# Kernel tuning notes

Measured on AMD Instinct MI355X. Metric: run time of the kernel, lower is better.

The kernel has to match this reference:

```python
import jax, jax.numpy as jnp
import numpy as np

N, D, E = 50000, 64, 800000  # nodes, node_dim, edges


def setup_inputs() -> dict:
    key = jax.random.key(0)
    ks = jax.random.split(key, 9)
    def lin(kw, fan_in, fan_out):
        # torch nn.Linear default init: U(-1/sqrt(fan_in), 1/sqrt(fan_in))
        bound = 1.0 / np.sqrt(fan_in)
        kw1, kw2 = jax.random.split(kw)
        W = jax.random.uniform(kw1, (fan_in, fan_out), jnp.float32, -bound, bound)
        b = jax.random.uniform(kw2, (fan_out,), jnp.float32, -bound, bound)
        return W, b
    W1, b1 = lin(ks[0], 2 * D + 2, D)
    W2, b2 = lin(ks[1], D, D // 2)
    W3, b3 = lin(ks[2], D // 2, D // 4)
    return {
        "node_features": jax.random.normal(ks[3], (N, D), jnp.float32),
        "edge_index": jax.random.randint(ks[4], (2, E), 0, N, jnp.int64),
        "spatial_features": jax.random.normal(ks[5], (E, 2), jnp.float32),
        "W1": W1, "b1": b1, "W2": W2, "b2": b2, "W3": W3, "b3": b3,
    }


def reference(node_features, edge_index, spatial_features, W1, b1, W2, b2, W3, b3):
    src = node_features[edge_index[0]]          # [E, D] gather
    dst = node_features[edge_index[1]]          # [E, D] gather
    x = jnp.concatenate([src, dst, spatial_features], axis=1)  # [E, 2D+2]
    h = jax.nn.relu(x @ W1 + b1)                # [E, D]
    h = jax.nn.relu(h @ W2 + b2)                # [E, D//2]
    return h @ W3 + b3                          # [E, D//4]
```

## Files before the change

kernel.cpp:

```cpp
#include <hip/hip_runtime.h>
#include <hip/hip_bf16.h>

#define NE 800000
#define NN 50000
#define TPW 4
#define NTILES (NE / 16)
#define NODE_TILES (NN / 16)

typedef __attribute__((ext_vector_type(8))) short        s16x8;
typedef __attribute__((ext_vector_type(8))) __bf16       bf16x8;
typedef __attribute__((ext_vector_type(4))) float        f32x4;
typedef __attribute__((ext_vector_type(2))) float        f32x2;
typedef __attribute__((ext_vector_type(4))) unsigned int u32x4;
typedef __attribute__((ext_vector_type(2))) unsigned int u32x2;

#define TAB_OFF 16384
#define WS_TAB ((size_t)(TAB_OFF + 2ull * NN * 64) * 2)
#define WS_NFB ((size_t)(TAB_OFF + 1ull * NN * 64) * 2)

__device__ __forceinline__ unsigned short f2bf_bits(float f) {
    __bf16 b = (__bf16)f;
    return __builtin_bit_cast(unsigned short, b);
}

__device__ __forceinline__ unsigned int pkbf(float a, float b) {
    return (unsigned int)f2bf_bits(a) | ((unsigned int)f2bf_bits(b) << 16);
}

__device__ __forceinline__ s16x8 cvt8(f32x4 a, f32x4 b) {
    bf16x8 r;
    r[0] = (__bf16)a[0]; r[1] = (__bf16)a[1]; r[2] = (__bf16)a[2]; r[3] = (__bf16)a[3];
    r[4] = (__bf16)b[0]; r[5] = (__bf16)b[1]; r[6] = (__bf16)b[2]; r[7] = (__bf16)b[3];
    return __builtin_bit_cast(s16x8, r);
}

__device__ __forceinline__ void ubf2(unsigned int u, float& lo, float& hi) {
    lo = __builtin_bit_cast(float, u << 16);
    hi = __builtin_bit_cast(float, u & 0xFFFF0000u);
}

__global__ void prep(const float* __restrict__ W1, const float* __restrict__ W2,
                     const float* __restrict__ W3, const float* __restrict__ nf,
                     unsigned short* __restrict__ ws, int do_nf) {
    unsigned short* w1t = ws;
    unsigned short* w2t = ws + 10240;
    unsigned short* w3t = ws + 12288;
    int t = blockIdx.x * blockDim.x + threadIdx.x;
    int stride = gridDim.x * blockDim.x;
    for (int i = t; i < 64 * 160; i += stride) {
        int j = i / 160, k = i % 160;
        w1t[i] = f2bf_bits(k < 130 ? W1[k * 64 + j] : 0.0f);
    }
    for (int i = t; i < 32 * 64; i += stride) {
        int j = i / 64, k = i % 64;
        w2t[i] = f2bf_bits(W2[k * 32 + j]);
    }
    for (int i = t; i < 16 * 32; i += stride) {
        int j = i / 32, k = i % 32;
        w3t[i] = f2bf_bits(W3[k * 16 + j]);
    }
    if (do_nf) {
        unsigned short* nfb = ws + TAB_OFF;
        for (int i = t; i < NN * 8; i += stride) {
            f32x4 a = *reinterpret_cast<const f32x4*>(nf + (long)i * 8);
            f32x4 b = *reinterpret_cast<const f32x4*>(nf + (long)i * 8 + 4);
            *reinterpret_cast<s16x8*>(nfb + (long)i * 8) = cvt8(a, b);
        }
    }
}

__global__ __launch_bounds__(256) void node_prep(
    const float* __restrict__ nf, const unsigned short* __restrict__ wsw,
    unsigned short* __restrict__ At, unsigned short* __restrict__ Bt) {
    const unsigned short* w1t = wsw;
    const int tid = threadIdx.x, wid = tid >> 6, lane = tid & 63;
    const int lr = lane & 15, lg = lane >> 4;

    s16x8 w1f[4][4];
    #pragma unroll
    for (int s = 0; s < 4; ++s)
        #pragma unroll
        for (int c = 0; c < 4; ++c)
            w1f[s][c] = *reinterpret_cast<const s16x8*>(w1t + (c * 16 + lr) * 160 + s * 32 + lg * 8);

    for (int tile = blockIdx.x * 4 + wid; tile < NODE_TILES; tile += gridDim.x * 4) {
        const int row = tile * 16 + lr;
        const float* p = nf + (long)row * 64;
        s16x8 nfr[2];
        #pragma unroll
        for (int s = 0; s < 2; ++s) {
            f32x4 a = *reinterpret_cast<const f32x4*>(p + s * 32 + lg * 8);
            f32x4 b = *reinterpret_cast<const f32x4*>(p + s * 32 + lg * 8 + 4);
            nfr[s] = cvt8(a, b);
        }
        f32x4 a4[4], b4[4];
        #pragma unroll
        for (int c = 0; c < 4; ++c) { a4[c] = (f32x4){0,0,0,0}; b4[c] = (f32x4){0,0,0,0}; }
        #pragma unroll
        for (int s = 0; s < 2; ++s)
            #pragma unroll
            for (int c = 0; c < 4; ++c) {
                a4[c] = __builtin_amdgcn_mfma_f32_16x16x32_bf16(w1f[s][c],     nfr[s], a4[c], 0, 0, 0);
                b4[c] = __builtin_amdgcn_mfma_f32_16x16x32_bf16(w1f[s + 2][c], nfr[s], b4[c], 0, 0, 0);
            }
        #pragma unroll
        for (int c = 0; c < 4; ++c) {
            u32x2 pa, pb;
            pa[0] = pkbf(a4[c][0], a4[c][1]); pa[1] = pkbf(a4[c][2], a4[c][3]);
            pb[0] = pkbf(b4[c][0], b4[c][1]); pb[1] = pkbf(b4[c][2], b4[c][3]);
            *reinterpret_cast<u32x2*>(At + (long)row * 64 + c * 16 + lg * 4) = pa;
            *reinterpret_cast<u32x2*>(Bt + (long)row * 64 + c * 16 + lg * 4) = pb;
        }
    }
}

__device__ __forceinline__ void gatherT(const unsigned short* At, const unsigned short* Bt,
                                        int si, int di, int lg, s16x8 g[4]) {
    const unsigned short* pa = At + (size_t)si * 64 + lg * 8;
    const unsigned short* pb = Bt + (size_t)di * 64 + lg * 8;
    g[0] = *reinterpret_cast<const s16x8*>(pa);
    g[1] = *reinterpret_cast<const s16x8*>(pa + 32);
    g[2] = *reinterpret_cast<const s16x8*>(pb);
    g[3] = *reinterpret_cast<const s16x8*>(pb + 32);
}

__global__ __launch_bounds__(256) void edge_mlp_tab(
    const int* __restrict__ ei, const float* __restrict__ sp,
    const float* __restrict__ W1, const float* __restrict__ b1,
    const float* __restrict__ b2, const float* __restrict__ b3,
    const unsigned short* __restrict__ wsw, float* __restrict__ out) {

    const unsigned short* w2t = wsw + 10240;
    const unsigned short* w3t = wsw + 12288;
    const unsigned short* At  = wsw + TAB_OFF;
    const unsigned short* Bt  = At + (size_t)NN * 64;

    __shared__ unsigned short h2s[4 * 16 * 40];

    const int tid = threadIdx.x, wid = tid >> 6, lane = tid & 63;
    const int lr = lane & 15, lg = lane >> 4;

    s16x8 w2f[2][2], w3f;
    #pragma unroll
    for (int s = 0; s < 2; ++s)
        #pragma unroll
        for (int c = 0; c < 2; ++c)
            w2f[s][c] = *reinterpret_cast<const s16x8*>(w2t + (c * 16 + lr) * 64 + s * 32 + lg * 8);
    w3f = *reinterpret_cast<const s16x8*>(w3t + lr * 32 + lg * 8);

    f32x4 b2v[2];
    #pragma unroll
    for (int c = 0; c < 2; ++c) b2v[c] = *reinterpret_cast<const f32x4*>(b2 + c * 16 + lg * 4);
    const f32x4 b3v = *reinterpret_cast<const f32x4*>(b3 + lg * 4);

    float c0f[2][8], c1f[2][8], cbf[2][8];
    #pragma unroll
    for (int jb = 0; jb < 2; ++jb) {
        const int j0 = jb * 32 + lg * 8;
        *reinterpret_cast<f32x4*>(&c0f[jb][0]) = *reinterpret_cast<const f32x4*>(W1 + 128 * 64 + j0);
        *reinterpret_cast<f32x4*>(&c0f[jb][4]) = *reinterpret_cast<const f32x4*>(W1 + 128 * 64 + j0 + 4);
        *reinterpret_cast<f32x4*>(&c1f[jb][0]) = *reinterpret_cast<const f32x4*>(W1 + 129 * 64 + j0);
        *reinterpret_cast<f32x4*>(&c1f[jb][4]) = *reinterpret_cast<const f32x4*>(W1 + 129 * 64 + j0 + 4);
        *reinterpret_cast<f32x4*>(&cbf[jb][0]) = *reinterpret_cast<const f32x4*>(b1 + j0);
        *reinterpret_cast<f32x4*>(&cbf[jb][4]) = *reinterpret_cast<const f32x4*>(b1 + j0 + 4);
    }

    const int tile0 = (blockIdx.x * 4 + wid) * TPW;
    int si[TPW], di[TPW];
    f32x2 spv[TPW];
    #pragma unroll
    for (int t = 0; t < TPW; ++t) {
        const int e = (tile0 + t) * 16 + lr;
        si[t] = ei[e];
        di[t] = ei[NE + e];
        spv[t] = *reinterpret_cast<const f32x2*>(sp + 2 * (size_t)e);
    }

    unsigned short* h2w = h2s + wid * (16 * 40) + lr * 40;

    s16x8 cur[4], nxt[4];
    gatherT(At, Bt, si[0], di[0], lg, cur);

    #pragma unroll
    for (int tt = 0; tt < TPW; ++tt) {
        if (tt + 1 < TPW)
            gatherT(At, Bt, si[tt + 1], di[tt + 1], lg, nxt);

        const float sp0 = spv[tt][0], sp1 = spv[tt][1];

        s16x8 bfr[2];
        #pragma unroll
        for (int jb = 0; jb < 2; ++jb) {
            u32x4 au = __builtin_bit_cast(u32x4, cur[jb]);
            u32x4 bu = __builtin_bit_cast(u32x4, cur[2 + jb]);
            u32x4 pk4;
            #pragma unroll
            for (int q = 0; q < 4; ++q) {
                float alo, ahi, blo, bhi;
                ubf2(au[q], alo, ahi);
                ubf2(bu[q], blo, bhi);
                float h0 = fmaf(sp0, c0f[jb][2 * q],
                           fmaf(sp1, c1f[jb][2 * q],     cbf[jb][2 * q]     + (alo + blo)));
                float h1 = fmaf(sp0, c0f[jb][2 * q + 1],
                           fmaf(sp1, c1f[jb][2 * q + 1], cbf[jb][2 * q + 1] + (ahi + bhi)));
                pk4[q] = pkbf(fmaxf(h0, 0.f), fmaxf(h1, 0.f));
            }
            bfr[jb] = __builtin_bit_cast(s16x8, pk4);
        }

        f32x4 acc2[2];
        #pragma unroll
        for (int c = 0; c < 2; ++c) acc2[c] = (f32x4){0, 0, 0, 0};
        #pragma unroll
        for (int s = 0; s < 2; ++s)
            #pragma unroll
            for (int c = 0; c < 2; ++c)
                acc2[c] = __builtin_amdgcn_mfma_f32_16x16x32_bf16(w2f[s][c], bfr[s], acc2[c], 0, 0, 0);

        #pragma unroll
        for (int c = 0; c < 2; ++c) {
            u32x2 p;
            p[0] = pkbf(fmaxf(acc2[c][0] + b2v[c][0], 0.f), fmaxf(acc2[c][1] + b2v[c][1], 0.f));
            p[1] = pkbf(fmaxf(acc2[c][2] + b2v[c][2], 0.f), fmaxf(acc2[c][3] + b2v[c][3], 0.f));
            *reinterpret_cast<u32x2*>(h2w + c * 16 + lg * 4) = p;
        }

        s16x8 bf3 = *reinterpret_cast<const s16x8*>(h2w + lg * 8);
        f32x4 acc3 = (f32x4){0, 0, 0, 0};
        acc3 = __builtin_amdgcn_mfma_f32_16x16x32_bf16(w3f, bf3, acc3, 0, 0, 0);

        f32x4 o;
        #pragma unroll
        for (int r = 0; r < 4; ++r) o[r] = acc3[r] + b3v[r];
        __builtin_nontemporal_store(o,
            reinterpret_cast<f32x4*>(out + (long)((tile0 + tt) * 16 + lr) * 16 + lg * 4));

        #pragma unroll
        for (int s = 0; s < 4; ++s) cur[s] = nxt[s];
    }
}

template <bool BF16NF>
__device__ __forceinline__ void gather4(const unsigned short* nfb, const float* nf,
                                        int si, int di, int lg, s16x8 g[4]) {
    if (BF16NF) {
        #pragma unroll
        for (int s = 0; s < 4; ++s) {
            const int row = (s < 2) ? si : di;
            g[s] = *reinterpret_cast<const s16x8*>(nfb + (long)row * 64 + (s & 1) * 32 + lg * 8);
        }
    } else {
        #pragma unroll
        for (int s = 0; s < 4; ++s) {
            const float* p = nf + (long)((s < 2) ? si : di) * 64 + (s & 1) * 32 + lg * 8;
            f32x4 a = *reinterpret_cast<const f32x4*>(p);
            f32x4 b = *reinterpret_cast<const f32x4*>(p + 4);
            g[s] = cvt8(a, b);
        }
    }
}

template <bool BF16NF>
__global__ __launch_bounds__(256) void edge_mlp_fb(
    const float* __restrict__ nf, const int* __restrict__ ei,
    const float* __restrict__ sp, const float* __restrict__ b1,
    const float* __restrict__ b2, const float* __restrict__ b3,
    const unsigned short* __restrict__ wsw, float* __restrict__ out) {

    const unsigned short* w1t = wsw;
    const unsigned short* w2t = wsw + 10240;
    const unsigned short* w3t = wsw + 12288;
    const unsigned short* nfb = wsw + TAB_OFF;

    __shared__ float h1s[4][16][68];
    __shared__ float h2s[4][16][36];

    const int tid = threadIdx.x, wid = tid >> 6, lane = tid & 63;
    const int lr = lane & 15, lg = lane >> 4;

    s16x8 w1f[5][4], w2f[2][2], w3f;
    #pragma unroll
    for (int s = 0; s < 5; ++s)
        #pragma unroll
        for (int c = 0; c < 4; ++c)
            w1f[s][c] = *reinterpret_cast<const s16x8*>(w1t + (c * 16 + lr) * 160 + s * 32 + lg * 8);
    #pragma unroll
    for (int s = 0; s < 2; ++s)
        #pragma unroll
        for (int c = 0; c < 2; ++c)
            w2f[s][c] = *reinterpret_cast<const s16x8*>(w2t + (c * 16 + lr) * 64 + s * 32 + lg * 8);
    w3f = *reinterpret_cast<const s16x8*>(w3t + lr * 32 + lg * 8);

    float bias1[4], bias2[2], bias3;
    #pragma unroll
    for (int c = 0; c < 4; ++c) bias1[c] = b1[c * 16 + lr];
    #pragma unroll
    for (int c = 0; c < 2; ++c) bias2[c] = b2[c * 16 + lr];
    bias3 = b3[lr];

    const int tile0 = (blockIdx.x * 4 + wid) * TPW;
    int si[TPW], di[TPW];
    f32x2 spv[TPW];
    #pragma unroll
    for (int t = 0; t < TPW; ++t) {
        const int e = (tile0 + t) * 16 + lr;
        si[t] = ei[e];
        di[t] = ei[NE + e];
        spv[t] = *reinterpret_cast<const f32x2*>(sp + 2 * (size_t)e);
    }

    s16x8 cur[4], nxt[4];
    gather4<BF16NF>(nfb, nf, si[0], di[0], lg, cur);

    #pragma unroll
    for (int tt = 0; tt < TPW; ++tt) {
        if (tt + 1 < TPW)
            gather4<BF16NF>(nfb, nf, si[tt + 1], di[tt + 1], lg, nxt);

        const int ebase = (tile0 + tt) * 16;

        f32x4 acc1[4];
        #pragma unroll
        for (int c = 0; c < 4; ++c) acc1[c] = (f32x4){0, 0, 0, 0};
        #pragma unroll
        for (int s = 0; s < 4; ++s)
            #pragma unroll
            for (int c = 0; c < 4; ++c)
                acc1[c] = __builtin_amdgcn_mfma_f32_16x16x32_bf16(cur[s], w1f[s][c], acc1[c], 0, 0, 0);
        {
            bf16x8 z;
            #pragma unroll
            for (int j = 0; j < 8; ++j) z[j] = (__bf16)0.0f;
            if (lg == 0) { z[0] = (__bf16)spv[tt][0]; z[1] = (__bf16)spv[tt][1]; }
            s16x8 af = __builtin_bit_cast(s16x8, z);
            #pragma unroll
            for (int c = 0; c < 4; ++c)
                acc1[c] = __builtin_amdgcn_mfma_f32_16x16x32_bf16(af, w1f[4][c], acc1[c], 0, 0, 0);
        }
        #pragma unroll
        for (int c = 0; c < 4; ++c)
            #pragma unroll
            for (int r = 0; r < 4; ++r)
                h1s[wid][lg * 4 + r][c * 16 + lr] = fmaxf(acc1[c][r] + bias1[c], 0.0f);

        f32x4 acc2[2];
        #pragma unroll
        for (int c = 0; c < 2; ++c) acc2[c] = (f32x4){0, 0, 0, 0};
        #pragma unroll
        for (int s = 0; s < 2; ++s) {
            f32x4 a = *reinterpret_cast<const f32x4*>(&h1s[wid][lr][s * 32 + lg * 8]);
            f32x4 b = *reinterpret_cast<const f32x4*>(&h1s[wid][lr][s * 32 + lg * 8 + 4]);
            s16x8 af = cvt8(a, b);
            #pragma unroll
            for (int c = 0; c < 2; ++c)
                acc2[c] = __builtin_amdgcn_mfma_f32_16x16x32_bf16(af, w2f[s][c], acc2[c], 0, 0, 0);
        }
        #pragma unroll
        for (int c = 0; c < 2; ++c)
            #pragma unroll
            for (int r = 0; r < 4; ++r)
                h2s[wid][lg * 4 + r][c * 16 + lr] = fmaxf(acc2[c][r] + bias2[c], 0.0f);

        f32x4 a3 = *reinterpret_cast<const f32x4*>(&h2s[wid][lr][lg * 8]);
        f32x4 b3x = *reinterpret_cast<const f32x4*>(&h2s[wid][lr][lg * 8 + 4]);
        s16x8 af3 = cvt8(a3, b3x);
        f32x4 acc3 = (f32x4){0, 0, 0, 0};
        acc3 = __builtin_amdgcn_mfma_f32_16x16x32_bf16(af3, w3f, acc3, 0, 0, 0);
        #pragma unroll
        for (int r = 0; r < 4; ++r)
            out[(long)(ebase + lg * 4 + r) * 16 + lr] = acc3[r] + bias3;

        #pragma unroll
        for (int s = 0; s < 4; ++s) cur[s] = nxt[s];
    }
}

extern "C" void kernel_launch(void* const* d_in, const int* in_sizes, int n_in,
                              void* d_out, int out_size, void* d_ws, size_t ws_size,
                              hipStream_t stream) {
    const float* nf = (const float*)d_in[0];
    const int*   ei = (const int*)d_in[1];
    const float* sp = (const float*)d_in[2];
    const float* W1 = (const float*)d_in[3];
    const float* b1 = (const float*)d_in[4];
    const float* W2 = (const float*)d_in[5];
    const float* b2 = (const float*)d_in[6];
    const float* W3 = (const float*)d_in[7];
    const float* b3 = (const float*)d_in[8];
    float* out = (float*)d_out;
    unsigned short* wsw = (unsigned short*)d_ws;

    const bool tab  = (ws_size >= WS_TAB);
    const bool bnfb = (!tab && ws_size >= WS_NFB);

    hipLaunchKernelGGL(prep, dim3(64), dim3(256), 0, stream,
                       W1, W2, W3, nf, wsw, bnfb ? 1 : 0);

    const int blocks = NTILES / TPW / 4;
    if (tab) {
        hipLaunchKernelGGL(node_prep, dim3(196), dim3(256), 0, stream,
                           nf, wsw, wsw + TAB_OFF, wsw + TAB_OFF + (size_t)NN * 64);
        hipLaunchKernelGGL(edge_mlp_tab, dim3(blocks), dim3(256), 0, stream,
                           ei, sp, W1, b1, b2, b3, wsw, out);
    } else if (bnfb) {
        hipLaunchKernelGGL(edge_mlp_fb<true>, dim3(blocks), dim3(256), 0, stream,
                           nf, ei, sp, b1, b2, b3, wsw, out);
    } else {
        hipLaunchKernelGGL(edge_mlp_fb<false>, dim3(blocks), dim3(256), 0, stream,
                           nf, ei, sp, b1, b2, b3, wsw, out);
    }
}
```

Baseline: 65.85 us.

## Fuse weight prep into node table kernel, fold bias, double-buffer edge index loads

The default table path drops the separate prep launch. The node-table kernel now reads and converts W1 fragments directly, and block 0 also transposes W2/W3. The layer-1 bias is folded into the source-node table, which removes a per-edge add. The edge kernel processes 8 tiles per wave with double-buffered index/spatial loads, nontemporal index loads, packed f32x2 math and alternating LDS scratch buffers. This saves one launch and some per-edge work, at the cost of fewer waves and more registers, plus a race risk because W2/W3 are written by block 0 in the same kernel but read only by the next kernel.

Result: slower. 77.59 us (+17.8%).

```diff
diff --git a/kernel.cpp b/kernel.cpp
--- a/kernel.cpp
+++ b/kernel.cpp
@@ -3,7 +3,7 @@
 
 #define NE 800000
 #define NN 50000
-#define TPW 4
+#define TPW 8
 #define NTILES (NE / 16)
 #define NODE_TILES (NN / 16)
 
@@ -34,9 +34,230 @@
     return __builtin_bit_cast(s16x8, r);
 }
 
-__device__ __forceinline__ void ubf2(unsigned int u, float& lo, float& hi) {
-    lo = __builtin_bit_cast(float, u << 16);
-    hi = __builtin_bit_cast(float, u & 0xFFFF0000u);
+__global__ __launch_bounds__(256) void node_prep_all(
+    const float* __restrict__ nf, const float* __restrict__ W1,
+    const float* __restrict__ b1, const float* __restrict__ W2,
+    const float* __restrict__ W3, unsigned short* __restrict__ ws) {
+    unsigned short* w2t = ws + 10240;
+    unsigned short* w3t = ws + 12288;
+    unsigned short* At  = ws + TAB_OFF;
+    unsigned short* Bt  = At + (size_t)NN * 64;
+
+    const int tid = threadIdx.x, wid = tid >> 6, lane = tid & 63;
+    const int lr = lane & 15, lg = lane >> 4;
+
+    if (blockIdx.x == 0) {
+        for (int i = tid; i < 32 * 64; i += 256) {
+            int j = i / 64, k = i % 64;
+            w2t[i] = f2bf_bits(W2[k * 32 + j]);
+        }
+        for (int i = tid; i < 16 * 32; i += 256) {
+            int j = i / 32, k = i % 32;
+            w3t[i] = f2bf_bits(W3[k * 16 + j]);
+        }
+    }
+
+    s16x8 w1f[4][4];
+    #pragma unroll
+    for (int s = 0; s < 4; ++s)
+        #pragma unroll
+        for (int c = 0; c < 4; ++c) {
+            bf16x8 w;
+            #pragma unroll
+            for (int b = 0; b < 8; ++b)
+                w[b] = (__bf16)W1[(s * 32 + lg * 8 + b) * 64 + c * 16 + lr];
+            w1f[s][c] = __builtin_bit_cast(s16x8, w);
+        }
+
+    f32x4 b1q[4];
+    #pragma unroll
+    for (int c = 0; c < 4; ++c)
+        b1q[c] = *reinterpret_cast<const f32x4*>(b1 + c * 16 + lg * 4);
+
+    for (int tile = blockIdx.x * 4 + wid; tile < NODE_TILES; tile += gridDim.x * 4) {
+        const int row = tile * 16 + lr;
+        const float* p = nf + (long)row * 64;
+        s16x8 nfr[2];
+        #pragma unroll
+        for (int s = 0; s < 2; ++s) {
+            f32x4 a = *reinterpret_cast<const f32x4*>(p + s * 32 + lg * 8);
+            f32x4 b = *reinterpret_cast<const f32x4*>(p + s * 32 + lg * 8 + 4);
+            nfr[s] = cvt8(a, b);
+        }
+        f32x4 a4[4], b4[4];
+        #pragma unroll
+        for (int c = 0; c < 4; ++c) { a4[c] = (f32x4){0,0,0,0}; b4[c] = (f32x4){0,0,0,0}; }
+        #pragma unroll
+        for (int s = 0; s < 2; ++s)
+            #pragma unroll
+            for (int c = 0; c < 4; ++c) {
+                a4[c] = __builtin_amdgcn_mfma_f32_16x16x32_bf16(w1f[s][c],     nfr[s], a4[c], 0, 0, 0);
+                b4[c] = __builtin_amdgcn_mfma_f32_16x16x32_bf16(w1f[s + 2][c], nfr[s], b4[c], 0, 0, 0);
+            }
+        #pragma unroll
+        for (int c = 0; c < 4; ++c) {
+            u32x2 pa, pb;
+            pa[0] = pkbf(a4[c][0] + b1q[c][0], a4[c][1] + b1q[c][1]);
+            pa[1] = pkbf(a4[c][2] + b1q[c][2], a4[c][3] + b1q[c][3]);
+            pb[0] = pkbf(b4[c][0], b4[c][1]);
+            pb[1] = pkbf(b4[c][2], b4[c][3]);
+            *reinterpret_cast<u32x2*>(At + (long)row * 64 + c * 16 + lg * 4) = pa;
+            *reinterpret_cast<u32x2*>(Bt + (long)row * 64 + c * 16 + lg * 4) = pb;
+        }
+    }
+}
+
+__device__ __forceinline__ void gatherT(const unsigned short* At, const unsigned short* Bt,
+                                        int si, int di, int lg, s16x8 g[4]) {
+    const unsigned short* pa = At + (size_t)si * 64 + lg * 8;
+    const unsigned short* pb = Bt + (size_t)di * 64 + lg * 8;
+    g[0] = *reinterpret_cast<const s16x8*>(pa);
+    g[1] = *reinterpret_cast<const s16x8*>(pa + 32);
+    g[2] = *reinterpret_cast<const s16x8*>(pb);
+    g[3] = *reinterpret_cast<const s16x8*>(pb + 32);
+}
+
+__device__ __forceinline__ void compute_tile(
+    int tile, const s16x8 cur[4], f32x2 s2,
+    const f32x2 c0p[2][4], const f32x2 c1p[2][4],
+    const s16x8 w2f[2][2], s16x8 w3f,
+    const f32x4 b2v[2], f32x4 b3v,
+    unsigned short* h2w, int lg, int lr, float* __restrict__ out) {
+
+    const f32x2 sp0v = {s2[0], s2[0]}, sp1v = {s2[1], s2[1]};
+
+    s16x8 bfr[2];
+    #pragma unroll
+    for (int jb = 0; jb < 2; ++jb) {
+        u32x4 au = __builtin_bit_cast(u32x4, cur[jb]);
+        u32x4 bu = __builtin_bit_cast(u32x4, cur[2 + jb]);
+        u32x4 pk4;
+        #pragma unroll
+        for (int q = 0; q < 4; ++q) {
+            f32x2 av = {__builtin_bit_cast(float, au[q] << 16),
+                        __builtin_bit_cast(float, au[q] & 0xFFFF0000u)};
+            f32x2 bv = {__builtin_bit_cast(float, bu[q] << 16),
+                        __builtin_bit_cast(float, bu[q] & 0xFFFF0000u)};
+            f32x2 h = av + bv;
+            h = sp1v * c1p[jb][q] + h;
+            h = sp0v * c0p[jb][q] + h;
+            pk4[q] = pkbf(fmaxf(h[0], 0.f), fmaxf(h[1], 0.f));
+        }
+        bfr[jb] = __builtin_bit_cast(s16x8, pk4);
+    }
+
+    f32x4 acc2[2];
+    #pragma unroll
+    for (int c = 0; c < 2; ++c) acc2[c] = (f32x4){0, 0, 0, 0};
+    #pragma unroll
+    for (int s = 0; s < 2; ++s)
+        #pragma unroll
+        for (int c = 0; c < 2; ++c)
+            acc2[c] = __builtin_amdgcn_mfma_f32_16x16x32_bf16(w2f[s][c], bfr[s], acc2[c], 0, 0, 0);
+
+    #pragma unroll
+    for (int c = 0; c < 2; ++c) {
+        u32x2 p;
+        p[0] = pkbf(fmaxf(acc2[c][0] + b2v[c][0], 0.f), fmaxf(acc2[c][1] + b2v[c][1], 0.f));
+        p[1] = pkbf(fmaxf(acc2[c][2] + b2v[c][2], 0.f), fmaxf(acc2[c][3] + b2v[c][3], 0.f));
+        *reinterpret_cast<u32x2*>(h2w + c * 16 + lg * 4) = p;
+    }
+
+    s16x8 bf3 = *reinterpret_cast<const s16x8*>(h2w + lg * 8);
+    f32x4 acc3 = (f32x4){0, 0, 0, 0};
+    acc3 = __builtin_amdgcn_mfma_f32_16x16x32_bf16(w3f, bf3, acc3, 0, 0, 0);
+
+    f32x4 o;
+    #pragma unroll
+    for (int r = 0; r < 4; ++r) o[r] = acc3[r] + b3v[r];
+    __builtin_nontemporal_store(o,
+        reinterpret_cast<f32x4*>(out + (long)(tile * 16 + lr) * 16 + lg * 4));
+}
+
+__global__ __launch_bounds__(256) void edge_mlp_tab(
+    const int* __restrict__ ei, const float* __restrict__ sp,
+    const float* __restrict__ W1, const float* __restrict__ b2,
+    const float* __restrict__ b3, const unsigned short* __restrict__ wsw,
+    float* __restrict__ out) {
+
+    const unsigned short* w2t = wsw + 10240;
+    const unsigned short* w3t = wsw + 12288;
+    const unsigned short* At  = wsw + TAB_OFF;
+    const unsigned short* Bt  = At + (size_t)NN * 64;
+
+    __shared__ unsigned short h2s[2][4 * 16 * 40];
+
+    const int tid = threadIdx.x, wid = tid >> 6, lane = tid & 63;
+    const int lr = lane & 15, lg = lane >> 4;
+
+    const int wgid  = blockIdx.x * 4 + wid;
+    const int tile0 = wgid * TPW;
+    if (tile0 >= NTILES) return;
+
+    s16x8 w2f[2][2], w3f;
+    #pragma unroll
+    for (int s = 0; s < 2; ++s)
+        #pragma unroll
+        for (int c = 0; c < 2; ++c)
+            w2f[s][c] = *reinterpret_cast<const s16x8*>(w2t + (c * 16 + lr) * 64 + s * 32 + lg * 8);
+    w3f = *reinterpret_cast<const s16x8*>(w3t + lr * 32 + lg * 8);
+
+    f32x4 b2v[2];
+    #pragma unroll
+    for (int c = 0; c < 2; ++c) b2v[c] = *reinterpret_cast<const f32x4*>(b2 + c * 16 + lg * 4);
+    const f32x4 b3v = *reinterpret_cast<const f32x4*>(b3 + lg * 4);
+
+    f32x2 c0p[2][4], c1p[2][4];
+    #pragma unroll
+    for (int jb = 0; jb < 2; ++jb) {
+        const int j0 = jb * 32 + lg * 8;
+        f32x4 x0 = *reinterpret_cast<const f32x4*>(W1 + 128 * 64 + j0);
+        f32x4 x1 = *reinterpret_cast<const f32x4*>(W1 + 128 * 64 + j0 + 4);
+        f32x4 y0 = *reinterpret_cast<const f32x4*>(W1 + 129 * 64 + j0);
+        f32x4 y1 = *reinterpret_cast<const f32x4*>(W1 + 129 * 64 + j0 + 4);
+        c0p[jb][0] = (f32x2){x0[0], x0[1]}; c0p[jb][1] = (f32x2){x0[2], x0[3]};
+        c0p[jb][2] = (f32x2){x1[0], x1[1]}; c0p[jb][3] = (f32x2){x1[2], x1[3]};
+        c1p[jb][0] = (f32x2){y0[0], y0[1]}; c1p[jb][1] = (f32x2){y0[2], y0[3]};
+        c1p[jb][2] = (f32x2){y1[0], y1[1]}; c1p[jb][3] = (f32x2){y1[2], y1[3]};
+    }
+
+    unsigned short* h2w0 = &h2s[0][wid * (16 * 40) + lr * 40];
+    unsigned short* h2w1 = &h2s[1][wid * (16 * 40) + lr * 40];
+
+    int sic[2][2], dic[2][2];
+    f32x2 spc[2][2];
+    #define LOADIDX(ck, bk)                                                          \
+        {                                                                            \
+            _Pragma("unroll") for (int v = 0; v < 2; ++v) {                          \
+                const size_t e = (size_t)(tile0 + (ck) * 2 + v) * 16 + lr;           \
+                sic[bk][v] = __builtin_nontemporal_load(ei + e);                     \
+                dic[bk][v] = __builtin_nontemporal_load(ei + NE + e);                \
+                spc[bk][v] = __builtin_nontemporal_load(                             \
+                    reinterpret_cast<const f32x2*>(sp) + e);                         \
+            }                                                                        \
+        }
+
+    LOADIDX(0, 0);
+    s16x8 cur[4], nxt[4];
+    gatherT(At, Bt, sic[0][0], dic[0][0], lg, cur);
+
+    #pragma unroll
+    for (int c = 0; c < TPW / 2; ++c) {
+        if (c + 1 < TPW / 2) { LOADIDX(c + 1, (c + 1) & 1); }
+        #pragma unroll
+        for (int u = 0; u < 2; ++u) {
+            const int t = c * 2 + u;
+            if (t + 1 < TPW) {
+                const int nb = ((t + 1) >> 1) & 1, nv = (t + 1) & 1;
+                gatherT(At, Bt, sic[nb][nv], dic[nb][nv], lg, nxt);
+            }
+            compute_tile(tile0 + t, cur, spc[c & 1][u], c0p, c1p, w2f, w3f,
+                         b2v, b3v, (u == 0) ? h2w0 : h2w1, lg, lr, out);
+            #pragma unroll
+            for (int s = 0; s < 4; ++s) cur[s] = nxt[s];
+        }
+    }
+    #undef LOADIDX
 }
 
 __global__ void prep(const float* __restrict__ W1, const float* __restrict__ W2,
@@ -69,177 +290,6 @@
     }
 }
 
-__global__ __launch_bounds__(256) void node_prep(
-    const float* __restrict__ nf, const unsigned short* __restrict__ wsw,
-    unsigned short* __restrict__ At, unsigned short* __restrict__ Bt) {
-    const unsigned short* w1t = wsw;
-    const int tid = threadIdx.x, wid = tid >> 6, lane = tid & 63;
-    const int lr = lane & 15, lg = lane >> 4;
-
-    s16x8 w1f[4][4];
-    #pragma unroll
-    for (int s = 0; s < 4; ++s)
-        #pragma unroll
-        for (int c = 0; c < 4; ++c)
-            w1f[s][c] = *reinterpret_cast<const s16x8*>(w1t + (c * 16 + lr) * 160 + s * 32 + lg * 8);
-
-    for (int tile = blockIdx.x * 4 + wid; tile < NODE_TILES; tile += gridDim.x * 4) {
-        const int row = tile * 16 + lr;
-        const float* p = nf + (long)row * 64;
-        s16x8 nfr[2];
-        #pragma unroll
-        for (int s = 0; s < 2; ++s) {
-            f32x4 a = *reinterpret_cast<const f32x4*>(p + s * 32 + lg * 8);
-            f32x4 b = *reinterpret_cast<const f32x4*>(p + s * 32 + lg * 8 + 4);
-            nfr[s] = cvt8(a, b);
-        }
-        f32x4 a4[4], b4[4];
-        #pragma unroll
-        for (int c = 0; c < 4; ++c) { a4[c] = (f32x4){0,0,0,0}; b4[c] = (f32x4){0,0,0,0}; }
-        #pragma unroll
-        for (int s = 0; s < 2; ++s)
-            #pragma unroll
-            for (int c = 0; c < 4; ++c) {
-                a4[c] = __builtin_amdgcn_mfma_f32_16x16x32_bf16(w1f[s][c],     nfr[s], a4[c], 0, 0, 0);
-                b4[c] = __builtin_amdgcn_mfma_f32_16x16x32_bf16(w1f[s + 2][c], nfr[s], b4[c], 0, 0, 0);
-            }
-        #pragma unroll
-        for (int c = 0; c < 4; ++c) {
-            u32x2 pa, pb;
-            pa[0] = pkbf(a4[c][0], a4[c][1]); pa[1] = pkbf(a4[c][2], a4[c][3]);
-            pb[0] = pkbf(b4[c][0], b4[c][1]); pb[1] = pkbf(b4[c][2], b4[c][3]);
-            *reinterpret_cast<u32x2*>(At + (long)row * 64 + c * 16 + lg * 4) = pa;
-            *reinterpret_cast<u32x2*>(Bt + (long)row * 64 + c * 16 + lg * 4) = pb;
-        }
-    }
-}
-
-__device__ __forceinline__ void gatherT(const unsigned short* At, const unsigned short* Bt,
-                                        int si, int di, int lg, s16x8 g[4]) {
-    const unsigned short* pa = At + (size_t)si * 64 + lg * 8;
-    const unsigned short* pb = Bt + (size_t)di * 64 + lg * 8;
-    g[0] = *reinterpret_cast<const s16x8*>(pa);
-    g[1] = *reinterpret_cast<const s16x8*>(pa + 32);
-    g[2] = *reinterpret_cast<const s16x8*>(pb);
-    g[3] = *reinterpret_cast<const s16x8*>(pb + 32);
-}
-
-__global__ __launch_bounds__(256) void edge_mlp_tab(
-    const int* __restrict__ ei, const float* __restrict__ sp,
-    const float* __restrict__ W1, const float* __restrict__ b1,
-    const float* __restrict__ b2, const float* __restrict__ b3,
-    const unsigned short* __restrict__ wsw, float* __restrict__ out) {
-
-    const unsigned short* w2t = wsw + 10240;
-    const unsigned short* w3t = wsw + 12288;
-    const unsigned short* At  = wsw + TAB_OFF;
-    const unsigned short* Bt  = At + (size_t)NN * 64;
-
-    __shared__ unsigned short h2s[4 * 16 * 40];
-
-    const int tid = threadIdx.x, wid = tid >> 6, lane = tid & 63;
-    const int lr = lane & 15, lg = lane >> 4;
-
-    s16x8 w2f[2][2], w3f;
-    #pragma unroll
-    for (int s = 0; s < 2; ++s)
-        #pragma unroll
-        for (int c = 0; c < 2; ++c)
-            w2f[s][c] = *reinterpret_cast<const s16x8*>(w2t + (c * 16 + lr) * 64 + s * 32 + lg * 8);
-    w3f = *reinterpret_cast<const s16x8*>(w3t + lr * 32 + lg * 8);
-
-    f32x4 b2v[2];
-    #pragma unroll
-    for (int c = 0; c < 2; ++c) b2v[c] = *reinterpret_cast<const f32x4*>(b2 + c * 16 + lg * 4);
-    const f32x4 b3v = *reinterpret_cast<const f32x4*>(b3 + lg * 4);
-
-    float c0f[2][8], c1f[2][8], cbf[2][8];
-    #pragma unroll
-    for (int jb = 0; jb < 2; ++jb) {
-        const int j0 = jb * 32 + lg * 8;
-        *reinterpret_cast<f32x4*>(&c0f[jb][0]) = *reinterpret_cast<const f32x4*>(W1 + 128 * 64 + j0);
-        *reinterpret_cast<f32x4*>(&c0f[jb][4]) = *reinterpret_cast<const f32x4*>(W1 + 128 * 64 + j0 + 4);
-        *reinterpret_cast<f32x4*>(&c1f[jb][0]) = *reinterpret_cast<const f32x4*>(W1 + 129 * 64 + j0);
-        *reinterpret_cast<f32x4*>(&c1f[jb][4]) = *reinterpret_cast<const f32x4*>(W1 + 129 * 64 + j0 + 4);
-        *reinterpret_cast<f32x4*>(&cbf[jb][0]) = *reinterpret_cast<const f32x4*>(b1 + j0);
-        *reinterpret_cast<f32x4*>(&cbf[jb][4]) = *reinterpret_cast<const f32x4*>(b1 + j0 + 4);
-    }
-
-    const int tile0 = (blockIdx.x * 4 + wid) * TPW;
-    int si[TPW], di[TPW];
-    f32x2 spv[TPW];
-    #pragma unroll
-    for (int t = 0; t < TPW; ++t) {
-        const int e = (tile0 + t) * 16 + lr;
-        si[t] = ei[e];
-        di[t] = ei[NE + e];
-        spv[t] = *reinterpret_cast<const f32x2*>(sp + 2 * (size_t)e);
-    }
-
-    unsigned short* h2w = h2s + wid * (16 * 40) + lr * 40;
-
-    s16x8 cur[4], nxt[4];
-    gatherT(At, Bt, si[0], di[0], lg, cur);
-
-    #pragma unroll
-    for (int tt = 0; tt < TPW; ++tt) {
-        if (tt + 1 < TPW)
-            gatherT(At, Bt, si[tt + 1], di[tt + 1], lg, nxt);
-
-        const float sp0 = spv[tt][0], sp1 = spv[tt][1];
-
-        s16x8 bfr[2];
-        #pragma unroll
-        for (int jb = 0; jb < 2; ++jb) {
-            u32x4 au = __builtin_bit_cast(u32x4, cur[jb]);
-            u32x4 bu = __builtin_bit_cast(u32x4, cur[2 + jb]);
-            u32x4 pk4;
-            #pragma unroll
-            for (int q = 0; q < 4; ++q) {
-                float alo, ahi, blo, bhi;
-                ubf2(au[q], alo, ahi);
-                ubf2(bu[q], blo, bhi);
-                float h0 = fmaf(sp0, c0f[jb][2 * q],
-                           fmaf(sp1, c1f[jb][2 * q],     cbf[jb][2 * q]     + (alo + blo)));
-                float h1 = fmaf(sp0, c0f[jb][2 * q + 1],
-                           fmaf(sp1, c1f[jb][2 * q + 1], cbf[jb][2 * q + 1] + (ahi + bhi)));
-                pk4[q] = pkbf(fmaxf(h0, 0.f), fmaxf(h1, 0.f));
-            }
-            bfr[jb] = __builtin_bit_cast(s16x8, pk4);
-        }
-
-        f32x4 acc2[2];
-        #pragma unroll
-        for (int c = 0; c < 2; ++c) acc2[c] = (f32x4){0, 0, 0, 0};
-        #pragma unroll
-        for (int s = 0; s < 2; ++s)
-            #pragma unroll
-            for (int c = 0; c < 2; ++c)
-                acc2[c] = __builtin_amdgcn_mfma_f32_16x16x32_bf16(w2f[s][c], bfr[s], acc2[c], 0, 0, 0);
-
-        #pragma unroll
-        for (int c = 0; c < 2; ++c) {
-            u32x2 p;
-            p[0] = pkbf(fmaxf(acc2[c][0] + b2v[c][0], 0.f), fmaxf(acc2[c][1] + b2v[c][1], 0.f));
-            p[1] = pkbf(fmaxf(acc2[c][2] + b2v[c][2], 0.f), fmaxf(acc2[c][3] + b2v[c][3], 0.f));
-            *reinterpret_cast<u32x2*>(h2w + c * 16 + lg * 4) = p;
-        }
-
-        s16x8 bf3 = *reinterpret_cast<const s16x8*>(h2w + lg * 8);
-        f32x4 acc3 = (f32x4){0, 0, 0, 0};
-        acc3 = __builtin_amdgcn_mfma_f32_16x16x32_bf16(w3f, bf3, acc3, 0, 0, 0);
-
-        f32x4 o;
-        #pragma unroll
-        for (int r = 0; r < 4; ++r) o[r] = acc3[r] + b3v[r];
-        __builtin_nontemporal_store(o,
-            reinterpret_cast<f32x4*>(out + (long)((tile0 + tt) * 16 + lr) * 16 + lg * 4));
-
-        #pragma unroll
-        for (int s = 0; s < 4; ++s) cur[s] = nxt[s];
-    }
-}
-
 template <bool BF16NF>
 __device__ __forceinline__ void gather4(const unsigned short* nfb, const float* nf,
                                         int si, int di, int lg, s16x8 g[4]) {
@@ -298,11 +348,11 @@
     for (int c = 0; c < 2; ++c) bias2[c] = b2[c * 16 + lr];
     bias3 = b3[lr];
 
-    const int tile0 = (blockIdx.x * 4 + wid) * TPW;
-    int si[TPW], di[TPW];
-    f32x2 spv[TPW];
-    #pragma unroll
-    for (int t = 0; t < TPW; ++t) {
+    const int tile0 = (blockIdx.x * 4 + wid) * 4;
+    int si[4], di[4];
+    f32x2 spv[4];
+    #pragma unroll
+    for (int t = 0; t < 4; ++t) {
         const int e = (tile0 + t) * 16 + lr;
         si[t] = ei[e];
         di[t] = ei[NE + e];
@@ -313,8 +363,8 @@
     gather4<BF16NF>(nfb, nf, si[0], di[0], lg, cur);
 
     #pragma unroll
-    for (int tt = 0; tt < TPW; ++tt) {
-        if (tt + 1 < TPW)
+    for (int tt = 0; tt < 4; ++tt) {
+        if (tt + 1 < 4)
             gather4<BF16NF>(nfb, nf, si[tt + 1], di[tt + 1], lg, nxt);
 
         const int ebase = (tile0 + tt) * 16;
@@ -393,20 +443,22 @@
     const bool tab  = (ws_size >= WS_TAB);
     const bool bnfb = (!tab && ws_size >= WS_NFB);
 
-    hipLaunchKernelGGL(prep, dim3(64), dim3(256), 0, stream,
-                       W1, W2, W3, nf, wsw, bnfb ? 1 : 0);
-
-    const int blocks = NTILES / TPW / 4;
     if (tab) {
-        hipLaunchKernelGGL(node_prep, dim3(196), dim3(256), 0, stream,
-                           nf, wsw, wsw + TAB_OFF, wsw + TAB_OFF + (size_t)NN * 64);
+        hipLaunchKernelGGL(node_prep_all, dim3(784), dim3(256), 0, stream,
+                           nf, W1, b1, W2, W3, wsw);
+        const int waves  = NTILES / TPW;
+        const int blocks = (waves + 3) / 4;
         hipLaunchKernelGGL(edge_mlp_tab, dim3(blocks), dim3(256), 0, stream,
-                           ei, sp, W1, b1, b2, b3, wsw, out);
-    } else if (bnfb) {
-        hipLaunchKernelGGL(edge_mlp_fb<true>, dim3(blocks), dim3(256), 0, stream,
-                           nf, ei, sp, b1, b2, b3, wsw, out);
+                           ei, sp, W1, b2, b3, wsw, out);
     } else {
-        hipLaunchKernelGGL(edge_mlp_fb<false>, dim3(blocks), dim3(256), 0, stream,
-                           nf, ei, sp, b1, b2, b3, wsw, out);
-    }
-}
+        hipLaunchKernelGGL(prep, dim3(64), dim3(256), 0, stream,
+                           W1, W2, W3, nf, wsw, bnfb ? 1 : 0);
+        const int blocks = NTILES / 4 / 4;
+        if (bnfb)
+            hipLaunchKernelGGL(edge_mlp_fb<true>, dim3(blocks), dim3(256), 0, stream,
+                               nf, ei, sp, b1, b2, b3, wsw, out);
+        else
+            hipLaunchKernelGGL(edge_mlp_fb<false>, dim3(blocks), dim3(256), 0, stream,
+                               nf, ei, sp, b1, b2, b3, wsw, out);
+    }
+}
```
